# Optimization experiments

Measured on AMD Instinct MI355X. Metric: run time of the kernel, lower is better.

Reference implementation:

```python
import jax, jax.numpy as jnp
import numpy as np

D_MODEL = 1024
N_HEADS = 16
HEAD_DIM = D_MODEL // N_HEADS


def setup_inputs() -> dict:
    key = jax.random.key(0)
    k1, k2, k3 = jax.random.split(key, 3)
    x = jax.random.normal(k1, (4, 2048, D_MODEL), dtype=jnp.float32)
    # torch Linear(d, 3d, bias=False): y = x @ W.T ; store transposed weight [d, 3d]
    scale = 1.0 / np.sqrt(D_MODEL)
    W_qkv = jax.random.normal(k2, (D_MODEL, 3 * D_MODEL), dtype=jnp.float32) * scale
    W_proj = jax.random.normal(k3, (D_MODEL, D_MODEL), dtype=jnp.float32) * scale
    return {"x": x, "W_qkv": W_qkv, "W_proj": W_proj}


def reference(x, W_qkv, W_proj):
    B, T, C = x.shape
    h, d = N_HEADS, HEAD_DIM
    qkv = x @ W_qkv                      # [B,T,3C]
    q, k, v = jnp.split(qkv, 3, axis=-1)
    def split_heads(t):
        return t.reshape(B, T, h, d).transpose(0, 2, 1, 3)  # [B,h,T,d]
    q, k, v = map(split_heads, (q, k, v))
    att = jnp.einsum('bhqd,bhkd->bhqk', q, k) / np.sqrt(d)  # [B,h,T,T]
    causal = jnp.tril(jnp.ones((T, T), dtype=bool))
    att = jnp.where(causal, att, -jnp.inf)
    att = jax.nn.softmax(att, axis=-1)
    # dropout = 0.0 (eval mode): no-op
    y = jnp.einsum('bhqk,bhkd->bhqd', att, v)               # [B,h,T,d]
    y = y.transpose(0, 2, 1, 3).reshape(B, T, C)
    return y @ W_proj
```

## Files before the change

kernel.cpp:

```cpp
#include <hip/hip_runtime.h>

#define T_SEQ 2048
#define D_MODEL 1024
#define NB 4
#define NH 16
#define HD 64

typedef __attribute__((ext_vector_type(8))) __bf16 bf16x8;
typedef __attribute__((ext_vector_type(4))) __bf16 bf16x4;
typedef __attribute__((ext_vector_type(4))) float f32x4;

__device__ __forceinline__ void gload_lds16(const void* g, void* l) {
  __builtin_amdgcn_global_load_lds((const __attribute__((address_space(1))) unsigned int*)g,
                                   (__attribute__((address_space(3))) unsigned int*)l,
                                   16, 0, 0);
}

__device__ __forceinline__ unsigned int pack_bf16_2(float e0, float e1) {
  unsigned short u0 = __builtin_bit_cast(unsigned short, (__bf16)e0);
  unsigned short u1 = __builtin_bit_cast(unsigned short, (__bf16)e1);
  return (unsigned int)u0 | ((unsigned int)u1 << 16);
}

__global__ __launch_bounds__(256) void cvt_bf16_kernel(const float* __restrict__ s,
                                                       __bf16* __restrict__ d, int n) {
  int i = (blockIdx.x * 256 + threadIdx.x) * 8;
  if (i >= n) return;
  float4 a = *(const float4*)(s + i);
  float4 b = *(const float4*)(s + i + 4);
  bf16x8 v;
  v[0] = (__bf16)a.x; v[1] = (__bf16)a.y; v[2] = (__bf16)a.z; v[3] = (__bf16)a.w;
  v[4] = (__bf16)b.x; v[5] = (__bf16)b.y; v[6] = (__bf16)b.z; v[7] = (__bf16)b.w;
  *(bf16x8*)(d + i) = v;
}

__global__ __launch_bounds__(256) void transpose_cvt_kernel(const float* __restrict__ W,
                                                            __bf16* __restrict__ Wt,
                                                            int K, int N) {
  __shared__ float t[32][33];
  int tx = threadIdx.x, ty = threadIdx.y;
  int n0 = blockIdx.x * 32, k0 = blockIdx.y * 32;
#pragma unroll
  for (int r = 0; r < 4; ++r)
    t[ty + r * 8][tx] = W[(size_t)(k0 + ty + r * 8) * N + n0 + tx];
  __syncthreads();
#pragma unroll
  for (int r = 0; r < 4; ++r)
    Wt[(size_t)(n0 + ty + r * 8) * K + k0 + tx] = (__bf16)t[tx][ty + r * 8];
}

__global__ __launch_bounds__(256) void extract_vt_kernel(const __bf16* __restrict__ qkv,
                                                         __bf16* __restrict__ Vt) {
  __shared__ __bf16 t[32][34];
  int tx = threadIdx.x, ty = threadIdx.y;
  int tt = blockIdx.x * 32;
  int dt = blockIdx.y * 32;
  int bh = blockIdx.z;
  int b = bh >> 4, h = bh & 15;
#pragma unroll
  for (int r = 0; r < 4; ++r)
    t[ty + r * 8][tx] = qkv[(size_t)(b * T_SEQ + tt + ty + r * 8) * 3072 + 2048 + h * HD + dt + tx];
  __syncthreads();
#pragma unroll
  for (int r = 0; r < 4; ++r)
    Vt[(size_t)(bh * HD + dt + ty + r * 8) * T_SEQ + tt + tx] = t[tx][ty + r * 8];
}

template <typename OutT>
__global__ __launch_bounds__(256) void gemm_bt(const __bf16* __restrict__ A,
                                               const __bf16* __restrict__ Bt,
                                               OutT* __restrict__ C,
                                               int M, int N, int K) {
  __shared__ __bf16 lA[128 * 64];
  __shared__ __bf16 lB[128 * 64];
  int tid = threadIdx.x;
  int lane = tid & 63, w = tid >> 6;
  int wm = w >> 1, wn = w & 1;
  int bn = blockIdx.x, bm = blockIdx.y;
  f32x4 acc[4][4] = {};
  for (int kt = 0; kt < K; kt += 64) {
#pragma unroll
    for (int it = 0; it < 4; ++it) {
      int o = it * 4096 + tid * 16;
      int row = o >> 7;
      int ss = ((o >> 4) & 7) ^ (row & 7);
      gload_lds16(A + (size_t)(bm * 128 + row) * K + kt + ss * 8, (char*)lA + o);
      gload_lds16(Bt + (size_t)(bn * 128 + row) * K + kt + ss * 8, (char*)lB + o);
    }
    __syncthreads();
    bf16x8 af[4][2], bfv[4][2];
#pragma unroll
    for (int i = 0; i < 4; ++i)
#pragma unroll
      for (int kk = 0; kk < 2; ++kk) {
        int ra = wm * 64 + i * 16 + (lane & 15);
        int sa = ((lane >> 4) + kk * 4) ^ (ra & 7);
        af[i][kk] = *(const bf16x8*)((const char*)lA + ra * 128 + sa * 16);
        int rb = wn * 64 + i * 16 + (lane & 15);
        int sb = ((lane >> 4) + kk * 4) ^ (rb & 7);
        bfv[i][kk] = *(const bf16x8*)((const char*)lB + rb * 128 + sb * 16);
      }
#pragma unroll
    for (int kk = 0; kk < 2; ++kk)
#pragma unroll
      for (int i = 0; i < 4; ++i)
#pragma unroll
        for (int j = 0; j < 4; ++j)
          acc[i][j] = __builtin_amdgcn_mfma_f32_16x16x32_bf16(af[i][kk], bfv[j][kk], acc[i][j], 0, 0, 0);
    __syncthreads();
  }
#pragma unroll
  for (int i = 0; i < 4; ++i)
#pragma unroll
    for (int j = 0; j < 4; ++j)
#pragma unroll
      for (int r = 0; r < 4; ++r) {
        int row = bm * 128 + wm * 64 + i * 16 + (lane >> 4) * 4 + r;
        int col = bn * 128 + wn * 64 + j * 16 + (lane & 15);
        C[(size_t)row * N + col] = (OutT)acc[i][j][r];
      }
}

__global__ __launch_bounds__(256) void attn_kernel(const __bf16* __restrict__ qkv,
                                                   const __bf16* __restrict__ Vt,
                                                   __bf16* __restrict__ Y) {
  __shared__ __bf16 lK[2][64 * 64];
  __shared__ __bf16 lV[2][64 * 64];
  int tid = threadIdx.x, lane = tid & 63, w = tid >> 6;
  int q = lane & 15, g = lane >> 4;

  int l = blockIdx.x;
  int j0 = l >> 3;
  int pair = ((l & 7) << 3) | (j0 >> 4);
  int p = j0 & 15;
  int h = pair & 15;
  int b = pair >> 4;

  const float SCALE = 0.125f * 1.44269504088896f;
  const f32x4 fzero = {0.f, 0.f, 0.f, 0.f};

#pragma unroll 1
  for (int pass = 0; pass < 2; ++pass) {
    int qt = pass ? p : 31 - p;

    const __bf16* qp = qkv + (size_t)(b * T_SEQ + qt * 64 + w * 16 + q) * 3072 + h * HD;
    bf16x8 qf[2];
    qf[0] = *(const bf16x8*)(qp + g * 8);
    qf[1] = *(const bf16x8*)(qp + 32 + g * 8);
#pragma unroll
    for (int kk = 0; kk < 2; ++kk)
#pragma unroll
      for (int jj = 0; jj < 8; ++jj) qf[kk][jj] = (__bf16)((float)qf[kk][jj] * SCALE);

    float m = -INFINITY, lsum = 0.f;
    f32x4 yacc[4];
#pragma unroll
    for (int f = 0; f < 4; ++f) yacc[f] = fzero;

    asm volatile("s_waitcnt vmcnt(0)" ::: "memory");
    __builtin_amdgcn_sched_barrier(0);

    auto STAGE = [&](int kvt, int bi) {
#pragma unroll
      for (int it = 0; it < 2; ++it) {
        int o = it * 4096 + tid * 16;
        int row = o >> 7;
        int ss = ((o >> 4) & 7) ^ (row & 7);
        gload_lds16(qkv + (size_t)(b * T_SEQ + kvt * 64 + row) * 3072 + 1024 + h * HD + ss * 8,
                    (char*)lK[bi] + o);
        gload_lds16(Vt + (size_t)((b * NH + h) * HD + row) * T_SEQ + kvt * 64 + ss * 8,
                    (char*)lV[bi] + o);
      }
    };

    STAGE(0, 0);

#pragma unroll 1
    for (int kvt = 0; kvt <= qt; ++kvt) {
      int cur = kvt & 1;
      if (kvt < qt) {
        STAGE(kvt + 1, cur ^ 1);
        asm volatile("s_waitcnt vmcnt(4)" ::: "memory");
      } else {
        asm volatile("s_waitcnt vmcnt(0)" ::: "memory");
      }
      __builtin_amdgcn_sched_barrier(0);
      __builtin_amdgcn_s_barrier();
      __builtin_amdgcn_sched_barrier(0);

      f32x4 s[4];
#pragma unroll
      for (int f = 0; f < 4; ++f) s[f] = fzero;
      const char* Kbase = (const char*)lK[cur];
      __builtin_amdgcn_s_setprio(1);
#pragma unroll
      for (int kk = 0; kk < 2; ++kk)
#pragma unroll
        for (int f = 0; f < 4; ++f) {
          int rk = f * 16 + q;
          int sk = (g + kk * 4) ^ (rk & 7);
          bf16x8 kf = *(const bf16x8*)(Kbase + rk * 128 + sk * 16);
          s[f] = __builtin_amdgcn_mfma_f32_16x16x32_bf16(kf, qf[kk], s[f], 0, 0, 0);
        }
      __builtin_amdgcn_s_setprio(0);

      if (kvt == qt) {
        int qloc = w * 16 + q;
#pragma unroll
        for (int f = 0; f < 4; ++f)
#pragma unroll
          for (int r = 0; r < 4; ++r)
            if (f * 16 + g * 4 + r > qloc) s[f][r] = -INFINITY;
      }
      float mx = fmaxf(fmaxf(fmaxf(s[0][0], s[0][1]), fmaxf(s[0][2], s[0][3])),
                       fmaxf(fmaxf(s[1][0], s[1][1]), fmaxf(s[1][2], s[1][3])));
      mx = fmaxf(mx, fmaxf(fmaxf(fmaxf(s[2][0], s[2][1]), fmaxf(s[2][2], s[2][3])),
                           fmaxf(fmaxf(s[3][0], s[3][1]), fmaxf(s[3][2], s[3][3]))));
      mx = fmaxf(mx, __shfl_xor(mx, 16, 64));
      mx = fmaxf(mx, __shfl_xor(mx, 32, 64));
      bool grew = mx > m;
      float alpha = 1.0f;
      if (grew) {
        alpha = exp2f(m - mx);
        m = mx;
        lsum *= alpha;
      }
      if (__any(grew)) {
#pragma unroll
        for (int r = 0; r < 4; ++r) {
          float ar = __shfl(alpha, g * 4 + r, 64);
#pragma unroll
          for (int f = 0; f < 4; ++f) yacc[f][r] *= ar;
        }
      }
      float ps = 0.f;
      unsigned int W[4][2];
#pragma unroll
      for (int f = 0; f < 4; ++f)
#pragma unroll
        for (int hh = 0; hh < 2; ++hh) {
          float e0 = exp2f(s[f][2 * hh] - m);
          float e1 = exp2f(s[f][2 * hh + 1] - m);
          ps += e0 + e1;
          W[f][hh] = pack_bf16_2(e0, e1);
        }
      lsum += ps;

      int srcA = ((g & 1) << 5) | q;
      int srcB = srcA + 16;
      bool hisel = (g >= 2);
      bf16x8 pa[2];
#pragma unroll
      for (int kk = 0; kk < 2; ++kk) {
        unsigned int pw[4];
#pragma unroll
        for (int t = 0; t < 4; ++t) {
          int src = (t < 2) ? srcA : srcB;
          unsigned int c0 = (unsigned int)__shfl((int)W[2 * kk][t & 1], src, 64);
          unsigned int c1 = (unsigned int)__shfl((int)W[2 * kk + 1][t & 1], src, 64);
          pw[t] = hisel ? c1 : c0;
        }
        uint4 u = make_uint4(pw[0], pw[1], pw[2], pw[3]);
        pa[kk] = __builtin_bit_cast(bf16x8, u);
      }

      const char* Vbase = (const char*)lV[cur];
      __builtin_amdgcn_s_setprio(1);
#pragma unroll
      for (int kk = 0; kk < 2; ++kk)
#pragma unroll
        for (int f = 0; f < 4; ++f) {
          int rv = f * 16 + q;
          int sv2 = (g + kk * 4) ^ (rv & 7);
          bf16x8 vf = *(const bf16x8*)(Vbase + rv * 128 + sv2 * 16);
          yacc[f] = __builtin_amdgcn_mfma_f32_16x16x32_bf16(pa[kk], vf, yacc[f], 0, 0, 0);
        }
      __builtin_amdgcn_s_setprio(0);

      __builtin_amdgcn_sched_barrier(0);
      asm volatile("s_waitcnt lgkmcnt(0)" ::: "memory");
      __builtin_amdgcn_s_barrier();
      __builtin_amdgcn_sched_barrier(0);
    }

    float ls = lsum;
    ls += __shfl_xor(ls, 16, 64);
    ls += __shfl_xor(ls, 32, 64);
    float linv = 1.0f / ls;
    int qrow = qt * 64 + w * 16 + g * 4;
#pragma unroll
    for (int r = 0; r < 4; ++r) {
      float lr = __shfl(linv, g * 4 + r, 64);
#pragma unroll
      for (int f = 0; f < 4; ++f) {
        Y[(size_t)(b * T_SEQ + qrow + r) * D_MODEL + h * HD + f * 16 + q] =
            (__bf16)(yacc[f][r] * lr);
      }
    }
  }
}

extern "C" void kernel_launch(void* const* d_in, const int* in_sizes, int n_in,
                              void* d_out, int out_size, void* d_ws, size_t ws_size,
                              hipStream_t stream) {
  const float* x = (const float*)d_in[0];
  const float* Wqkv = (const float*)d_in[1];
  const float* Wproj = (const float*)d_in[2];
  float* out = (float*)d_out;
  char* ws = (char*)d_ws;

  __bf16* Xbf     = (__bf16*)(ws);
  __bf16* Wqkv_t  = (__bf16*)(ws + 16777216);
  __bf16* Wproj_t = (__bf16*)(ws + 23068672);
  __bf16* QKV     = (__bf16*)(ws + 25165824);
  __bf16* Vt      = (__bf16*)(ws + 75497472);
  __bf16* Yb      = (__bf16*)(ws + 92274688);

  cvt_bf16_kernel<<<4096, 256, 0, stream>>>(x, Xbf, NB * T_SEQ * D_MODEL);
  transpose_cvt_kernel<<<dim3(96, 32), dim3(32, 8), 0, stream>>>(Wqkv, Wqkv_t, 1024, 3072);
  transpose_cvt_kernel<<<dim3(32, 32), dim3(32, 8), 0, stream>>>(Wproj, Wproj_t, 1024, 1024);
  gemm_bt<__bf16><<<dim3(24, 64), 256, 0, stream>>>(Xbf, Wqkv_t, QKV, 8192, 3072, 1024);
  extract_vt_kernel<<<dim3(64, 2, 64), dim3(32, 8), 0, stream>>>(QKV, Vt);
  attn_kernel<<<1024, 256, 0, stream>>>(QKV, Vt, Yb);
  gemm_bt<float><<<dim3(8, 64), 256, 0, stream>>>(Yb, Wproj_t, out, 8192, 1024, 1024);
}
```

Measured before the change: 316.1 us.

## Give each attention wave two query sub-tiles and add lazy softmax rescaling

```diff
diff --git a/kernel.cpp b/kernel.cpp
--- a/kernel.cpp
+++ b/kernel.cpp
@@ -76,7 +76,11 @@
   int tid = threadIdx.x;
   int lane = tid & 63, w = tid >> 6;
   int wm = w >> 1, wn = w & 1;
-  int bn = blockIdx.x, bm = blockIdx.y;
+  int nwgx = gridDim.x;
+  int lid = blockIdx.y * nwgx + blockIdx.x;
+  int cpx = (nwgx * gridDim.y) >> 3;
+  int swz = (lid & 7) * cpx + (lid >> 3);
+  int bn = swz % nwgx, bm = swz / nwgx;
   f32x4 acc[4][4] = {};
   for (int kt = 0; kt < K; kt += 64) {
 #pragma unroll
@@ -121,7 +125,7 @@
       }
 }
 
-__global__ __launch_bounds__(256) void attn_kernel(const __bf16* __restrict__ qkv,
+__global__ __launch_bounds__(128) void attn_kernel(const __bf16* __restrict__ qkv,
                                                    const __bf16* __restrict__ Vt,
                                                    __bf16* __restrict__ Y) {
   __shared__ __bf16 lK[2][64 * 64];
@@ -130,11 +134,9 @@
   int q = lane & 15, g = lane >> 4;
 
   int l = blockIdx.x;
-  int j0 = l >> 3;
-  int pair = ((l & 7) << 3) | (j0 >> 4);
-  int p = j0 & 15;
-  int h = pair & 15;
-  int b = pair >> 4;
+  int pairHB = ((l & 7) << 3) | (l >> 7);
+  int p = (l >> 3) & 15;
+  int h = pairHB & 15, b = pairHB >> 4;
 
   const float SCALE = 0.125f * 1.44269504088896f;
   const f32x4 fzero = {0.f, 0.f, 0.f, 0.f};
@@ -143,27 +145,34 @@
   for (int pass = 0; pass < 2; ++pass) {
     int qt = pass ? p : 31 - p;
 
-    const __bf16* qp = qkv + (size_t)(b * T_SEQ + qt * 64 + w * 16 + q) * 3072 + h * HD;
-    bf16x8 qf[2];
-    qf[0] = *(const bf16x8*)(qp + g * 8);
-    qf[1] = *(const bf16x8*)(qp + 32 + g * 8);
-#pragma unroll
-    for (int kk = 0; kk < 2; ++kk)
-#pragma unroll
-      for (int jj = 0; jj < 8; ++jj) qf[kk][jj] = (__bf16)((float)qf[kk][jj] * SCALE);
-
-    float m = -INFINITY, lsum = 0.f;
-    f32x4 yacc[4];
-#pragma unroll
-    for (int f = 0; f < 4; ++f) yacc[f] = fzero;
+    bf16x8 qf[2][2];
+#pragma unroll
+    for (int qi = 0; qi < 2; ++qi) {
+      const __bf16* qp =
+          qkv + (size_t)(b * T_SEQ + qt * 64 + w * 32 + qi * 16 + q) * 3072 + h * HD;
+      qf[qi][0] = *(const bf16x8*)(qp + g * 8);
+      qf[qi][1] = *(const bf16x8*)(qp + 32 + g * 8);
+#pragma unroll
+      for (int kk = 0; kk < 2; ++kk)
+#pragma unroll
+        for (int jj = 0; jj < 8; ++jj)
+          qf[qi][kk][jj] = (__bf16)((float)qf[qi][kk][jj] * SCALE);
+    }
+
+    float m[2] = {-INFINITY, -INFINITY}, lsum[2] = {0.f, 0.f};
+    f32x4 yacc[2][4];
+#pragma unroll
+    for (int qi = 0; qi < 2; ++qi)
+#pragma unroll
+      for (int f = 0; f < 4; ++f) yacc[qi][f] = fzero;
 
     asm volatile("s_waitcnt vmcnt(0)" ::: "memory");
     __builtin_amdgcn_sched_barrier(0);
 
     auto STAGE = [&](int kvt, int bi) {
 #pragma unroll
-      for (int it = 0; it < 2; ++it) {
-        int o = it * 4096 + tid * 16;
+      for (int it = 0; it < 4; ++it) {
+        int o = it * 2048 + tid * 16;
         int row = o >> 7;
         int ss = ((o >> 4) & 7) ^ (row & 7);
         gload_lds16(qkv + (size_t)(b * T_SEQ + kvt * 64 + row) * 3072 + 1024 + h * HD + ss * 8,
@@ -180,7 +189,7 @@
       int cur = kvt & 1;
       if (kvt < qt) {
         STAGE(kvt + 1, cur ^ 1);
-        asm volatile("s_waitcnt vmcnt(4)" ::: "memory");
+        asm volatile("s_waitcnt vmcnt(8)" ::: "memory");
       } else {
         asm volatile("s_waitcnt vmcnt(0)" ::: "memory");
       }
@@ -188,9 +197,11 @@
       __builtin_amdgcn_s_barrier();
       __builtin_amdgcn_sched_barrier(0);
 
-      f32x4 s[4];
-#pragma unroll
-      for (int f = 0; f < 4; ++f) s[f] = fzero;
+      f32x4 s[2][4];
+#pragma unroll
+      for (int qi = 0; qi < 2; ++qi)
+#pragma unroll
+        for (int f = 0; f < 4; ++f) s[qi][f] = fzero;
       const char* Kbase = (const char*)lK[cur];
       __builtin_amdgcn_s_setprio(1);
 #pragma unroll
@@ -200,69 +211,88 @@
           int rk = f * 16 + q;
           int sk = (g + kk * 4) ^ (rk & 7);
           bf16x8 kf = *(const bf16x8*)(Kbase + rk * 128 + sk * 16);
-          s[f] = __builtin_amdgcn_mfma_f32_16x16x32_bf16(kf, qf[kk], s[f], 0, 0, 0);
+#pragma unroll
+          for (int qi = 0; qi < 2; ++qi)
+            s[qi][f] = __builtin_amdgcn_mfma_f32_16x16x32_bf16(kf, qf[qi][kk], s[qi][f], 0, 0, 0);
         }
       __builtin_amdgcn_s_setprio(0);
 
       if (kvt == qt) {
-        int qloc = w * 16 + q;
+#pragma unroll
+        for (int qi = 0; qi < 2; ++qi) {
+          int qloc = w * 32 + qi * 16 + q;
+#pragma unroll
+          for (int f = 0; f < 4; ++f)
+#pragma unroll
+            for (int r = 0; r < 4; ++r)
+              if (f * 16 + g * 4 + r > qloc) s[qi][f][r] = -INFINITY;
+        }
+      }
+
+      float mx[2];
+#pragma unroll
+      for (int qi = 0; qi < 2; ++qi) {
+        float v = fmaxf(fmaxf(fmaxf(s[qi][0][0], s[qi][0][1]), fmaxf(s[qi][0][2], s[qi][0][3])),
+                        fmaxf(fmaxf(s[qi][1][0], s[qi][1][1]), fmaxf(s[qi][1][2], s[qi][1][3])));
+        v = fmaxf(v, fmaxf(fmaxf(fmaxf(s[qi][2][0], s[qi][2][1]), fmaxf(s[qi][2][2], s[qi][2][3])),
+                           fmaxf(fmaxf(s[qi][3][0], s[qi][3][1]), fmaxf(s[qi][3][2], s[qi][3][3]))));
+        v = fmaxf(v, __shfl_xor(v, 16, 64));
+        v = fmaxf(v, __shfl_xor(v, 32, 64));
+        mx[qi] = v;
+      }
+
+      float growth = fmaxf(mx[0] - m[0], mx[1] - m[1]);
+      if (__any(growth > 8.0f)) {
+#pragma unroll
+        for (int qi = 0; qi < 2; ++qi) {
+          float mn = fmaxf(m[qi], mx[qi]);
+          float al = exp2f(m[qi] - mn);
+          m[qi] = mn;
+          lsum[qi] *= al;
+#pragma unroll
+          for (int r = 0; r < 4; ++r) {
+            float ar = __shfl(al, g * 4 + r, 64);
+#pragma unroll
+            for (int f = 0; f < 4; ++f) yacc[qi][f][r] *= ar;
+          }
+        }
+      }
+
+      unsigned int Wd[2][4][2];
+#pragma unroll
+      for (int qi = 0; qi < 2; ++qi) {
+        float ps = 0.f;
 #pragma unroll
         for (int f = 0; f < 4; ++f)
 #pragma unroll
-          for (int r = 0; r < 4; ++r)
-            if (f * 16 + g * 4 + r > qloc) s[f][r] = -INFINITY;
-      }
-      float mx = fmaxf(fmaxf(fmaxf(s[0][0], s[0][1]), fmaxf(s[0][2], s[0][3])),
-                       fmaxf(fmaxf(s[1][0], s[1][1]), fmaxf(s[1][2], s[1][3])));
-      mx = fmaxf(mx, fmaxf(fmaxf(fmaxf(s[2][0], s[2][1]), fmaxf(s[2][2], s[2][3])),
-                           fmaxf(fmaxf(s[3][0], s[3][1]), fmaxf(s[3][2], s[3][3]))));
-      mx = fmaxf(mx, __shfl_xor(mx, 16, 64));
-      mx = fmaxf(mx, __shfl_xor(mx, 32, 64));
-      bool grew = mx > m;
-      float alpha = 1.0f;
-      if (grew) {
-        alpha = exp2f(m - mx);
-        m = mx;
-        lsum *= alpha;
-      }
-      if (__any(grew)) {
-#pragma unroll
-        for (int r = 0; r < 4; ++r) {
-          float ar = __shfl(alpha, g * 4 + r, 64);
-#pragma unroll
-          for (int f = 0; f < 4; ++f) yacc[f][r] *= ar;
-        }
-      }
-      float ps = 0.f;
-      unsigned int W[4][2];
-#pragma unroll
-      for (int f = 0; f < 4; ++f)
-#pragma unroll
-        for (int hh = 0; hh < 2; ++hh) {
-          float e0 = exp2f(s[f][2 * hh] - m);
-          float e1 = exp2f(s[f][2 * hh + 1] - m);
-          ps += e0 + e1;
-          W[f][hh] = pack_bf16_2(e0, e1);
-        }
-      lsum += ps;
+          for (int hh = 0; hh < 2; ++hh) {
+            float e0 = exp2f(s[qi][f][2 * hh] - m[qi]);
+            float e1 = exp2f(s[qi][f][2 * hh + 1] - m[qi]);
+            ps += e0 + e1;
+            Wd[qi][f][hh] = pack_bf16_2(e0, e1);
+          }
+        lsum[qi] += ps;
+      }
 
       int srcA = ((g & 1) << 5) | q;
       int srcB = srcA + 16;
       bool hisel = (g >= 2);
-      bf16x8 pa[2];
-#pragma unroll
-      for (int kk = 0; kk < 2; ++kk) {
-        unsigned int pw[4];
-#pragma unroll
-        for (int t = 0; t < 4; ++t) {
-          int src = (t < 2) ? srcA : srcB;
-          unsigned int c0 = (unsigned int)__shfl((int)W[2 * kk][t & 1], src, 64);
-          unsigned int c1 = (unsigned int)__shfl((int)W[2 * kk + 1][t & 1], src, 64);
-          pw[t] = hisel ? c1 : c0;
-        }
-        uint4 u = make_uint4(pw[0], pw[1], pw[2], pw[3]);
-        pa[kk] = __builtin_bit_cast(bf16x8, u);
-      }
+      bf16x8 pa[2][2];
+#pragma unroll
+      for (int qi = 0; qi < 2; ++qi)
+#pragma unroll
+        for (int kk = 0; kk < 2; ++kk) {
+          unsigned int pw[4];
+#pragma unroll
+          for (int t = 0; t < 4; ++t) {
+            int src = (t < 2) ? srcA : srcB;
+            unsigned int c0 = (unsigned int)__shfl((int)Wd[qi][2 * kk][t & 1], src, 64);
+            unsigned int c1 = (unsigned int)__shfl((int)Wd[qi][2 * kk + 1][t & 1], src, 64);
+            pw[t] = hisel ? c1 : c0;
+          }
+          uint4 u = make_uint4(pw[0], pw[1], pw[2], pw[3]);
+          pa[qi][kk] = __builtin_bit_cast(bf16x8, u);
+        }
 
       const char* Vbase = (const char*)lV[cur];
       __builtin_amdgcn_s_setprio(1);
@@ -273,7 +303,9 @@
           int rv = f * 16 + q;
           int sv2 = (g + kk * 4) ^ (rv & 7);
           bf16x8 vf = *(const bf16x8*)(Vbase + rv * 128 + sv2 * 16);
-          yacc[f] = __builtin_amdgcn_mfma_f32_16x16x32_bf16(pa[kk], vf, yacc[f], 0, 0, 0);
+#pragma unroll
+          for (int qi = 0; qi < 2; ++qi)
+            yacc[qi][f] = __builtin_amdgcn_mfma_f32_16x16x32_bf16(pa[qi][kk], vf, yacc[qi][f], 0, 0, 0);
         }
       __builtin_amdgcn_s_setprio(0);
 
@@ -283,18 +315,21 @@
       __builtin_amdgcn_sched_barrier(0);
     }
 
-    float ls = lsum;
-    ls += __shfl_xor(ls, 16, 64);
-    ls += __shfl_xor(ls, 32, 64);
-    float linv = 1.0f / ls;
-    int qrow = qt * 64 + w * 16 + g * 4;
-#pragma unroll
-    for (int r = 0; r < 4; ++r) {
-      float lr = __shfl(linv, g * 4 + r, 64);
-#pragma unroll
-      for (int f = 0; f < 4; ++f) {
-        Y[(size_t)(b * T_SEQ + qrow + r) * D_MODEL + h * HD + f * 16 + q] =
-            (__bf16)(yacc[f][r] * lr);
+#pragma unroll
+    for (int qi = 0; qi < 2; ++qi) {
+      float ls = lsum[qi];
+      ls += __shfl_xor(ls, 16, 64);
+      ls += __shfl_xor(ls, 32, 64);
+      float linv = 1.0f / ls;
+      int qrow = qt * 64 + w * 32 + qi * 16 + g * 4;
+#pragma unroll
+      for (int r = 0; r < 4; ++r) {
+        float lr = __shfl(linv, g * 4 + r, 64);
+#pragma unroll
+        for (int f = 0; f < 4; ++f) {
+          Y[(size_t)(b * T_SEQ + qrow + r) * D_MODEL + h * HD + f * 16 + q] =
+              (__bf16)(yacc[qi][f][r] * lr);
+        }
       }
     }
   }
@@ -321,6 +356,6 @@
   transpose_cvt_kernel<<<dim3(32, 32), dim3(32, 8), 0, stream>>>(Wproj, Wproj_t, 1024, 1024);
   gemm_bt<__bf16><<<dim3(24, 64), 256, 0, stream>>>(Xbf, Wqkv_t, QKV, 8192, 3072, 1024);
   extract_vt_kernel<<<dim3(64, 2, 64), dim3(32, 8), 0, stream>>>(QKV, Vt);
-  attn_kernel<<<1024, 256, 0, stream>>>(QKV, Vt, Yb);
+  attn_kernel<<<1024, 128, 0, stream>>>(QKV, Vt, Yb);
   gemm_bt<float><<<dim3(8, 64), 256, 0, stream>>>(Yb, Wproj_t, out, 8192, 1024, 1024);
 }
```

Measured after the change: 299.7 us. 1.05x faster.
